# Kernel tuning notes

Measured on AMD Instinct MI355X. Metric: run time of the kernel, lower is better.

## Reference

```python
import jax, jax.numpy as jnp
import numpy as np

B, S, H, I, E, K = 2, 2048, 1024, 2816, 8, 2


def setup_inputs() -> dict:
    key = jax.random.key(0)
    k1, k2, k3, k4, k5 = jax.random.split(key, 5)
    std = 0.02
    x = jax.random.normal(k1, (B, S, H), dtype=jnp.float32)
    gate_w = jax.random.normal(k2, (H, E), dtype=jnp.float32) * std   # router Linear(H,E), no bias
    Wg = jax.random.normal(k3, (E, H, I), dtype=jnp.float32) * std    # per-expert gate_proj
    Wu = jax.random.normal(k4, (E, H, I), dtype=jnp.float32) * std    # per-expert up_proj
    Wd = jax.random.normal(k5, (E, I, H), dtype=jnp.float32) * std    # per-expert down_proj
    return {"x": x, "gate_w": gate_w, "Wg": Wg, "Wu": Wu, "Wd": Wd}


def reference(x, gate_w, Wg, Wu, Wd):
    b, s, h = x.shape
    e = gate_w.shape[1]
    # --- Gating ---
    logits = jnp.einsum('bsh,he->bse', x, gate_w)                      # [B,S,E]
    top_vals, top_idx = jax.lax.top_k(logits, K)                       # [B,S,K]
    sel = (top_idx[..., None] == jnp.arange(e)).any(axis=-2)           # [B,S,E] bool, top-k mask
    sparse_logits = jnp.where(sel, logits, -jnp.inf)
    sparse_probs = jax.nn.softmax(sparse_logits, axis=-1)              # zero weight off top-k
    # --- Experts (dense over E, weighted by sparse probs; math identical to gather/scatter loop) ---
    xf = x.reshape(-1, h)                                              # [T,H], T=B*S
    g = jnp.einsum('th,ehi->tei', xf, Wg)                              # [T,E,I]
    u = jnp.einsum('th,ehi->tei', xf, Wu)
    act = jax.nn.silu(g) * u                                           # SwiGLU
    expert_out = jnp.einsum('tei,eih->teh', act, Wd)                   # [T,E,H]
    out = jnp.einsum('teh,te->th', expert_out, sparse_probs.reshape(-1, e))
    final_outputs = out.reshape(b, s, h)
    gate_logit = logits.reshape(-1, e)                                 # [B*S,E]
    return final_outputs, gate_logit
```

## Files before the change

### kernel.cpp

```cpp
#include <hip/hip_runtime.h>


namespace {
constexpr int TOKS = 4096;
constexpr int HDIM = 1024;
constexpr int IDIM = 2816;
constexpr int NEXP = 8;
constexpr int NROW = 8192;
constexpr int MTILES = 72;

constexpr size_t WGT_OFF = 0;
constexpr size_t WUT_OFF = 46137344;
constexpr size_t WDT_OFF = 92274688;
constexpr size_t A_OFF   = 138412032;
constexpr size_t ACT_OFF = 155189248;
constexpr size_t CNT_OFF = 201326592;
constexpr size_t TIX_OFF = CNT_OFF + 1024;
constexpr size_t TPR_OFF = CNT_OFF + 66560;
constexpr size_t PRT_OFF = 0;
}

typedef __attribute__((ext_vector_type(8))) short short8;
typedef __attribute__((ext_vector_type(8))) unsigned short ushort8;
typedef __attribute__((ext_vector_type(4))) float f32x4;

__device__ __forceinline__ unsigned short f2bf(float f) {
  union { float f; unsigned int u; } v; v.f = f;
  unsigned int u = v.u;
  return (unsigned short)((u + 0x7fffu + ((u >> 16) & 1u)) >> 16);
}

__device__ __forceinline__ void gl2lds16(const void* g, void* l) {
  __builtin_amdgcn_global_load_lds(
      (const __attribute__((address_space(1))) void*)g,
      (__attribute__((address_space(3))) void*)l, 16, 0, 0);
}

__device__ __forceinline__ void tile_map(const int* __restrict__ cnt, int y,
                                         int& e, int& m0, int& off, int& ne) {
  e = -1; m0 = 0; off = 0; ne = 0;
  int s = 0;
#pragma unroll
  for (int ee = 0; ee < NEXP; ++ee) {
    int c = cnt[ee];
    int nt = (c + 127) >> 7;
    if (e < 0) {
      if (y < nt) { e = ee; m0 = y << 7; off = s; ne = c; }
      else y -= nt;
    }
    s += c;
  }
}

__global__ __launch_bounds__(256) void k_transpose_all(
    const float* __restrict__ Wg, const float* __restrict__ Wu,
    const float* __restrict__ Wd, unsigned short* __restrict__ WgT,
    unsigned short* __restrict__ WuT, unsigned short* __restrict__ WdT,
    int* __restrict__ cnt) {
  const int z = blockIdx.z;
  if (z == 0 && blockIdx.x == 0 && threadIdx.x < NEXP) cnt[threadIdx.x] = 0;
  const float* in; unsigned short* out; int C, R;
  if (z < 8)       { in = Wg; out = WgT; C = IDIM; R = HDIM; }
  else if (z < 16) { in = Wu; out = WuT; C = IDIM; R = HDIM; }
  else             { in = Wd; out = WdT; C = HDIM; R = IDIM; }
  const size_t eoff = (size_t)(z & 7) * HDIM * IDIM;
  in += eoff; out += eoff;
  const int nbx = C / 64;
  const int c0 = (blockIdx.x % nbx) * 64, r0 = (blockIdx.x / nbx) * 64;
  __shared__ float tile[64][65];
  const int tid = threadIdx.x;
  const int rr = tid >> 4, cc4 = (tid & 15) * 4;
#pragma unroll
  for (int i = 0; i < 4; ++i) {
    int r = rr + i * 16;
    float4 v = *(const float4*)(in + (size_t)(r0 + r) * C + c0 + cc4);
    tile[r][cc4 + 0] = v.x; tile[r][cc4 + 1] = v.y;
    tile[r][cc4 + 2] = v.z; tile[r][cc4 + 3] = v.w;
  }
  __syncthreads();
  const int j = tid & 7;
#pragma unroll
  for (int i = 0; i < 2; ++i) {
    int c = (tid >> 3) + i * 32;
    ushort8 o;
#pragma unroll
    for (int k = 0; k < 8; ++k) o[k] = f2bf(tile[j * 8 + k][c]);
    *(ushort8*)(out + (size_t)(c0 + c) * R + r0 + j * 8) = o;
  }
}

__global__ __launch_bounds__(256) void k_gating(
    const float* __restrict__ x, const float* __restrict__ gw,
    float* __restrict__ logits_out, int* __restrict__ cnt,
    int4* __restrict__ tidx, float2* __restrict__ tprb) {
  const int lane = threadIdx.x & 63;
  const int t = blockIdx.x * 4 + (threadIdx.x >> 6);
  const float4* xr = (const float4*)(x + (size_t)t * HDIM);
  double acc[8];
#pragma unroll
  for (int e = 0; e < 8; ++e) acc[e] = 0.0;
#pragma unroll
  for (int jj = 0; jj < 4; ++jj) {
    float4 xv = xr[lane + jj * 64];
    const int hb = (lane + jj * 64) * 4;
    const float xs[4] = {xv.x, xv.y, xv.z, xv.w};
#pragma unroll
    for (int c = 0; c < 4; ++c) {
      const float4* g = (const float4*)(gw + (size_t)(hb + c) * 8);
      float4 g0 = g[0], g1 = g[1];
      acc[0] += (double)xs[c] * g0.x; acc[1] += (double)xs[c] * g0.y;
      acc[2] += (double)xs[c] * g0.z; acc[3] += (double)xs[c] * g0.w;
      acc[4] += (double)xs[c] * g1.x; acc[5] += (double)xs[c] * g1.y;
      acc[6] += (double)xs[c] * g1.z; acc[7] += (double)xs[c] * g1.w;
    }
  }
#pragma unroll
  for (int off = 32; off > 0; off >>= 1) {
#pragma unroll
    for (int e = 0; e < 8; ++e) acc[e] += __shfl_down(acc[e], off);
  }
  if (lane == 0) {
    float lg[8];
#pragma unroll
    for (int e = 0; e < 8; ++e) lg[e] = (float)acc[e];
#pragma unroll
    for (int e = 0; e < 8; ++e) logits_out[(size_t)t * 8 + e] = lg[e];
    float v0 = lg[0]; int i0 = 0; float v1 = -3.0e38f; int i1 = 0;
#pragma unroll
    for (int e = 1; e < 8; ++e) {
      if (lg[e] > v0) { v1 = v0; i1 = i0; v0 = lg[e]; i0 = e; }
      else if (lg[e] > v1) { v1 = lg[e]; i1 = e; }
    }
    float ex = expf(v1 - v0);
    float p0 = 1.0f / (1.0f + ex);
    float p1 = ex / (1.0f + ex);
    int r0 = atomicAdd(&cnt[i0], 1);
    int r1 = atomicAdd(&cnt[i1], 1);
    tidx[t] = make_int4(i0, i1, r0, r1);
    tprb[t] = make_float2(p0, p1);
  }
}

__global__ __launch_bounds__(256) void k_build(
    const float* __restrict__ x, const int4* __restrict__ tidx,
    const int* __restrict__ cnt, unsigned short* __restrict__ A) {
  const int t = blockIdx.x;
  const int4 ii = tidx[t];
  int o0 = 0, o1 = 0;
#pragma unroll
  for (int e = 0; e < NEXP - 1; ++e) {
    int c = cnt[e];
    o0 += (e < ii.x) ? c : 0;
    o1 += (e < ii.y) ? c : 0;
  }
  const int r0 = o0 + ii.z, r1 = o1 + ii.w;
  float4 v = ((const float4*)(x + (size_t)t * HDIM))[threadIdx.x];
  ushort4 b;
  b.x = f2bf(v.x); b.y = f2bf(v.y); b.z = f2bf(v.z); b.w = f2bf(v.w);
  ((ushort4*)(A + (size_t)r0 * HDIM))[threadIdx.x] = b;
  ((ushort4*)(A + (size_t)r1 * HDIM))[threadIdx.x] = b;
}

__global__ __launch_bounds__(256, 4) void k_gemm1(
    const unsigned short* __restrict__ A, const unsigned short* __restrict__ WgT,
    const unsigned short* __restrict__ WuT, unsigned short* __restrict__ act,
    const int* __restrict__ cnt) {
  int e, m0, off, ne;
  tile_map(cnt, blockIdx.y, e, m0, off, ne);
  if (e < 0) return;
  const int n0 = blockIdx.x * 64;
  const unsigned short* Bg = WgT + ((size_t)e * IDIM + n0) * HDIM;
  const unsigned short* Bu = WuT + ((size_t)e * IDIM + n0) * HDIM;

  __shared__ unsigned short As[128 * 64];
  __shared__ unsigned short Bgs[64 * 64];
  __shared__ unsigned short Bus[64 * 64];

  const int tid = threadIdx.x, w = tid >> 6, lane = tid & 63;
  const int lrow8 = lane >> 3;
  const int swz = ((lane & 7) ^ lrow8) * 8;
  const int m16 = lane & 15, quad = lane >> 4, l7 = lane & 7;

  f32x4 accg[2][4], accu[2][4];
#pragma unroll
  for (int mi = 0; mi < 2; ++mi)
#pragma unroll
    for (int ni = 0; ni < 4; ++ni) {
      accg[mi][ni] = (f32x4){0.f, 0.f, 0.f, 0.f};
      accu[mi][ni] = (f32x4){0.f, 0.f, 0.f, 0.f};
    }

  for (int kt = 0; kt < HDIM / 64; ++kt) {
    const int k0 = kt * 64;
#pragma unroll
    for (int i = 0; i < 4; ++i) {
      int gr = off + m0 + w * 32 + i * 8 + lrow8;
      gr = gr > (NROW - 1) ? (NROW - 1) : gr;
      gl2lds16(A + (size_t)gr * HDIM + k0 + swz, &As[(w * 32 + i * 8) * 64]);
    }
#pragma unroll
    for (int i = 0; i < 2; ++i) {
      int rl = w * 16 + i * 8 + lrow8;
      gl2lds16(Bg + (size_t)rl * HDIM + k0 + swz, &Bgs[(w * 16 + i * 8) * 64]);
      gl2lds16(Bu + (size_t)rl * HDIM + k0 + swz, &Bus[(w * 16 + i * 8) * 64]);
    }
    __syncthreads();
#pragma unroll
    for (int kk = 0; kk < 2; ++kk) {
      const int jc = ((kk * 4 + quad) ^ l7) * 8;
      short8 af[2], bgf[4], buf[4];
#pragma unroll
      for (int mi = 0; mi < 2; ++mi)
        af[mi] = *(const short8*)&As[(w * 32 + mi * 16 + m16) * 64 + jc];
#pragma unroll
      for (int ni = 0; ni < 4; ++ni) {
        bgf[ni] = *(const short8*)&Bgs[(ni * 16 + m16) * 64 + jc];
        buf[ni] = *(const short8*)&Bus[(ni * 16 + m16) * 64 + jc];
      }
#pragma unroll
      for (int mi = 0; mi < 2; ++mi)
#pragma unroll
        for (int ni = 0; ni < 4; ++ni) {
          accg[mi][ni] = __builtin_amdgcn_mfma_f32_16x16x32_bf16(
              af[mi], bgf[ni], accg[mi][ni], 0, 0, 0);
          accu[mi][ni] = __builtin_amdgcn_mfma_f32_16x16x32_bf16(
              af[mi], buf[ni], accu[mi][ni], 0, 0, 0);
        }
    }
    __syncthreads();
  }
#pragma unroll
  for (int mi = 0; mi < 2; ++mi)
#pragma unroll
    for (int ni = 0; ni < 4; ++ni)
#pragma unroll
      for (int r = 0; r < 4; ++r) {
        int ml = w * 32 + mi * 16 + quad * 4 + r;
        float g = accg[mi][ni][r];
        float u = accu[mi][ni][r];
        float s = g / (1.0f + __expf(-g));
        As[ml * 64 + ni * 16 + m16] = f2bf(s * u);
      }
  __syncthreads();
#pragma unroll
  for (int i = 0; i < 4; ++i) {
    int chunk = i * 256 + tid;
    int row = chunk >> 3, j = chunk & 7;
    if (m0 + row < ne)
      *(ushort8*)&act[(size_t)(off + m0 + row) * IDIM + n0 + j * 8] =
          *(const ushort8*)&As[row * 64 + j * 8];
  }
}

__global__ __launch_bounds__(256, 2) void k_gemm2(
    const unsigned short* __restrict__ act, const unsigned short* __restrict__ WdT,
    float* __restrict__ partial, const int* __restrict__ cnt) {
  int e, m0, off, ne;
  tile_map(cnt, blockIdx.y, e, m0, off, ne);
  if (e < 0) return;
  const int n0 = blockIdx.x * 128;
  const unsigned short* B = WdT + ((size_t)e * HDIM + n0) * IDIM;

  __shared__ unsigned short As[128 * 64];
  __shared__ unsigned short Bs[128 * 64];

  const int tid = threadIdx.x, w = tid >> 6, lane = tid & 63;
  const int lrow8 = lane >> 3;
  const int swz = ((lane & 7) ^ lrow8) * 8;
  const int m16 = lane & 15, quad = lane >> 4, l7 = lane & 7;
  const int wm = (w >> 1) * 64, wn = (w & 1) * 64;

  f32x4 acc[4][4];
#pragma unroll
  for (int mi = 0; mi < 4; ++mi)
#pragma unroll
    for (int ni = 0; ni < 4; ++ni) acc[mi][ni] = (f32x4){0.f, 0.f, 0.f, 0.f};

  for (int kt = 0; kt < IDIM / 64; ++kt) {
    const int k0 = kt * 64;
#pragma unroll
    for (int i = 0; i < 4; ++i) {
      int rl = w * 32 + i * 8 + lrow8;
      int gr = off + m0 + rl;
      gr = gr > (NROW - 1) ? (NROW - 1) : gr;
      gl2lds16(act + (size_t)gr * IDIM + k0 + swz, &As[(w * 32 + i * 8) * 64]);
      gl2lds16(B + (size_t)rl * IDIM + k0 + swz, &Bs[(w * 32 + i * 8) * 64]);
    }
    __syncthreads();
#pragma unroll
    for (int kk = 0; kk < 2; ++kk) {
      const int jc = ((kk * 4 + quad) ^ l7) * 8;
      short8 af[4], bf[4];
#pragma unroll
      for (int mi = 0; mi < 4; ++mi)
        af[mi] = *(const short8*)&As[(wm + mi * 16 + m16) * 64 + jc];
#pragma unroll
      for (int ni = 0; ni < 4; ++ni)
        bf[ni] = *(const short8*)&Bs[(wn + ni * 16 + m16) * 64 + jc];
#pragma unroll
      for (int mi = 0; mi < 4; ++mi)
#pragma unroll
        for (int ni = 0; ni < 4; ++ni)
          acc[mi][ni] = __builtin_amdgcn_mfma_f32_16x16x32_bf16(
              af[mi], bf[ni], acc[mi][ni], 0, 0, 0);
    }
    __syncthreads();
  }
#pragma unroll
  for (int mi = 0; mi < 4; ++mi)
#pragma unroll
    for (int ni = 0; ni < 4; ++ni)
#pragma unroll
      for (int r = 0; r < 4; ++r) {
        int ml = wm + mi * 16 + quad * 4 + r;
        if (m0 + ml < ne)
          partial[(size_t)(off + m0 + ml) * HDIM + n0 + wn + ni * 16 + m16] =
              acc[mi][ni][r];
      }
}

__global__ __launch_bounds__(256) void k_combine(
    const float* __restrict__ partial, const int4* __restrict__ tidx,
    const int* __restrict__ cnt, const float2* __restrict__ tprb,
    float* __restrict__ out) {
  const int t = blockIdx.x;
  const int4 ii = tidx[t];
  int o0 = 0, o1 = 0;
#pragma unroll
  for (int e = 0; e < NEXP - 1; ++e) {
    int c = cnt[e];
    o0 += (e < ii.x) ? c : 0;
    o1 += (e < ii.y) ? c : 0;
  }
  const int r0 = o0 + ii.z, r1 = o1 + ii.w;
  const float2 p = tprb[t];
  float4 a = ((const float4*)(partial + (size_t)r0 * HDIM))[threadIdx.x];
  float4 b = ((const float4*)(partial + (size_t)r1 * HDIM))[threadIdx.x];
  float4 o;
  o.x = p.x * a.x + p.y * b.x;
  o.y = p.x * a.y + p.y * b.y;
  o.z = p.x * a.z + p.y * b.z;
  o.w = p.x * a.w + p.y * b.w;
  ((float4*)(out + (size_t)t * HDIM))[threadIdx.x] = o;
}

extern "C" void kernel_launch(void* const* d_in, const int* in_sizes, int n_in,
                              void* d_out, int out_size, void* d_ws, size_t ws_size,
                              hipStream_t stream) {
  const float* x  = (const float*)d_in[0];
  const float* gw = (const float*)d_in[1];
  const float* Wg = (const float*)d_in[2];
  const float* Wu = (const float*)d_in[3];
  const float* Wd = (const float*)d_in[4];
  float* out = (float*)d_out;
  char* ws = (char*)d_ws;

  unsigned short* WgT = (unsigned short*)(ws + WGT_OFF);
  unsigned short* WuT = (unsigned short*)(ws + WUT_OFF);
  unsigned short* WdT = (unsigned short*)(ws + WDT_OFF);
  unsigned short* A   = (unsigned short*)(ws + A_OFF);
  unsigned short* act = (unsigned short*)(ws + ACT_OFF);
  float* partial = (float*)(ws + PRT_OFF);
  int* cnt  = (int*)(ws + CNT_OFF);
  int4* tidx = (int4*)(ws + TIX_OFF);
  float2* tprb = (float2*)(ws + TPR_OFF);

  float* logits_out = out + (size_t)TOKS * HDIM;

  k_transpose_all<<<dim3(704, 1, 24), 256, 0, stream>>>(Wg, Wu, Wd, WgT, WuT,
                                                        WdT, cnt);
  k_gating<<<TOKS / 4, 256, 0, stream>>>(x, gw, logits_out, cnt, tidx, tprb);
  k_build<<<TOKS, 256, 0, stream>>>(x, tidx, cnt, A);
  k_gemm1<<<dim3(IDIM / 64, MTILES), 256, 0, stream>>>(A, WgT, WuT, act, cnt);
  k_gemm2<<<dim3(HDIM / 128, MTILES), 256, 0, stream>>>(act, WdT, partial, cnt);
  k_combine<<<TOKS, 256, 0, stream>>>(partial, tidx, cnt, tprb, out);
}
```

Measured before the change: 591.2 us.

## Widen transpose tiles, add XCD-aware block swizzle to GEMMs, raise gemm2 occupancy

The weight transpose kernel now handles two 64-column tiles per block, issuing all eight global loads up front to raise memory-level parallelism, and the grid is halved to match. Both expert GEMMs remap the linear block id so that blocks landing on the same XCD (id mod 8) cover contiguous tiles, aiming for better L2 reuse of weights and activations. gemm2's launch bounds request 4 blocks per SM instead of 2, which may cause register spills.

```diff
diff --git a/kernel.cpp b/kernel.cpp
--- a/kernel.cpp
+++ b/kernel.cpp
@@ -65,28 +65,41 @@
   else             { in = Wd; out = WdT; C = HDIM; R = IDIM; }
   const size_t eoff = (size_t)(z & 7) * HDIM * IDIM;
   in += eoff; out += eoff;
-  const int nbx = C / 64;
-  const int c0 = (blockIdx.x % nbx) * 64, r0 = (blockIdx.x / nbx) * 64;
+  const int nbx = C / 128;
+  const int c0 = (blockIdx.x % nbx) * 128, r0 = (blockIdx.x / nbx) * 64;
   __shared__ float tile[64][65];
   const int tid = threadIdx.x;
   const int rr = tid >> 4, cc4 = (tid & 15) * 4;
-#pragma unroll
-  for (int i = 0; i < 4; ++i) {
-    int r = rr + i * 16;
-    float4 v = *(const float4*)(in + (size_t)(r0 + r) * C + c0 + cc4);
-    tile[r][cc4 + 0] = v.x; tile[r][cc4 + 1] = v.y;
-    tile[r][cc4 + 2] = v.z; tile[r][cc4 + 3] = v.w;
-  }
+
+  float4 v0[4], v1[4];
+#pragma unroll
+  for (int i = 0; i < 4; ++i)
+    v0[i] = *(const float4*)(in + (size_t)(r0 + rr + i * 16) * C + c0 + cc4);
+#pragma unroll
+  for (int i = 0; i < 4; ++i)
+    v1[i] = *(const float4*)(in + (size_t)(r0 + rr + i * 16) * C + c0 + 64 + cc4);
+
+  auto process = [&](const float4 (&v)[4], int cbase) {
+#pragma unroll
+    for (int i = 0; i < 4; ++i) {
+      int r = rr + i * 16;
+      tile[r][cc4 + 0] = v[i].x; tile[r][cc4 + 1] = v[i].y;
+      tile[r][cc4 + 2] = v[i].z; tile[r][cc4 + 3] = v[i].w;
+    }
+    __syncthreads();
+    const int j = tid & 7;
+#pragma unroll
+    for (int i = 0; i < 2; ++i) {
+      int c = (tid >> 3) + i * 32;
+      ushort8 o;
+#pragma unroll
+      for (int k = 0; k < 8; ++k) o[k] = f2bf(tile[j * 8 + k][c]);
+      *(ushort8*)(out + (size_t)(cbase + c) * R + r0 + j * 8) = o;
+    }
+  };
+  process(v0, c0);
   __syncthreads();
-  const int j = tid & 7;
-#pragma unroll
-  for (int i = 0; i < 2; ++i) {
-    int c = (tid >> 3) + i * 32;
-    ushort8 o;
-#pragma unroll
-    for (int k = 0; k < 8; ++k) o[k] = f2bf(tile[j * 8 + k][c]);
-    *(ushort8*)(out + (size_t)(c0 + c) * R + r0 + j * 8) = o;
-  }
+  process(v1, c0 + 64);
 }
 
 __global__ __launch_bounds__(256) void k_gating(
@@ -165,10 +178,13 @@
     const unsigned short* __restrict__ A, const unsigned short* __restrict__ WgT,
     const unsigned short* __restrict__ WuT, unsigned short* __restrict__ act,
     const int* __restrict__ cnt) {
+  const int orig = blockIdx.y * gridDim.x + blockIdx.x;
+  const int swz_id = (orig & 7) * 396 + (orig >> 3);
+  const int bx = swz_id / MTILES, by = swz_id % MTILES;
   int e, m0, off, ne;
-  tile_map(cnt, blockIdx.y, e, m0, off, ne);
+  tile_map(cnt, by, e, m0, off, ne);
   if (e < 0) return;
-  const int n0 = blockIdx.x * 64;
+  const int n0 = bx * 64;
   const unsigned short* Bg = WgT + ((size_t)e * IDIM + n0) * HDIM;
   const unsigned short* Bu = WuT + ((size_t)e * IDIM + n0) * HDIM;
 
@@ -252,13 +268,16 @@
   }
 }
 
-__global__ __launch_bounds__(256, 2) void k_gemm2(
+__global__ __launch_bounds__(256, 4) void k_gemm2(
     const unsigned short* __restrict__ act, const unsigned short* __restrict__ WdT,
     float* __restrict__ partial, const int* __restrict__ cnt) {
+  const int orig = blockIdx.y * gridDim.x + blockIdx.x;
+  const int swz_id = (orig & 7) * 72 + (orig >> 3);
+  const int bx = swz_id / MTILES, by = swz_id % MTILES;
   int e, m0, off, ne;
-  tile_map(cnt, blockIdx.y, e, m0, off, ne);
+  tile_map(cnt, by, e, m0, off, ne);
   if (e < 0) return;
-  const int n0 = blockIdx.x * 128;
+  const int n0 = bx * 128;
   const unsigned short* B = WdT + ((size_t)e * HDIM + n0) * IDIM;
 
   __shared__ unsigned short As[128 * 64];
@@ -367,7 +386,7 @@
 
   float* logits_out = out + (size_t)TOKS * HDIM;
 
-  k_transpose_all<<<dim3(704, 1, 24), 256, 0, stream>>>(Wg, Wu, Wd, WgT, WuT,
+  k_transpose_all<<<dim3(352, 1, 24), 256, 0, stream>>>(Wg, Wu, Wd, WgT, WuT,
                                                         WdT, cnt);
   k_gating<<<TOKS / 4, 256, 0, stream>>>(x, gw, logits_out, cnt, tidx, tprb);
   k_build<<<TOKS, 256, 0, stream>>>(x, tidx, cnt, A);
```

Result: slower. 606.6 us (+2.6%).
